# Kernel tuning notes

Measured on AMD Instinct MI355X. Metric: run time of the kernel, lower is better.

The kernel has to match this reference:

```python
import jax, jax.numpy as jnp
import numpy as np

B, T, H, L, OUT = 64, 2048, 256, 2, 256


def setup_inputs() -> dict:
    key = jax.random.key(0)
    ks = jax.random.split(key, 7)
    s = 1.0 / np.sqrt(H)
    return {
        "x": jax.random.normal(ks[0], (B, T, H), dtype=jnp.float32),
        "W_ih": jax.random.uniform(ks[1], (L, 4 * H, H), jnp.float32, -s, s),
        "W_hh": jax.random.uniform(ks[2], (L, 4 * H, H), jnp.float32, -s, s),
        "b_ih": jax.random.uniform(ks[3], (L, 4 * H), jnp.float32, -s, s),
        "b_hh": jax.random.uniform(ks[4], (L, 4 * H), jnp.float32, -s, s),
        "W_fc": jax.random.uniform(ks[5], (OUT, H), jnp.float32, -s, s),
        "b_fc": jax.random.uniform(ks[6], (OUT,), jnp.float32, -s, s),
    }


def _lstm_forward(x, W_ih, W_hh, b_ih, b_hh, W_fc, b_fc):
    n_layers = W_ih.shape[0]
    batch = x.shape[0]
    hidden = W_hh.shape[2]
    h0 = jnp.zeros((n_layers, batch, hidden), x.dtype)
    c0 = jnp.zeros((n_layers, batch, hidden), x.dtype)

    def step(carry, x_t):
        h, c = carry  # [L, B, H] each
        inp = x_t  # [B, in]
        new_h, new_c = [], []
        for l in range(n_layers):
            # gates: [B, 4H] = x W_ih^T + b_ih + h W_hh^T + b_hh
            gates = (inp @ W_ih[l].T + b_ih[l]) + (h[l] @ W_hh[l].T + b_hh[l])
            i_g, f_g, g_g, o_g = jnp.split(gates, 4, axis=-1)
            c_new = jax.nn.sigmoid(f_g) * c[l] + jax.nn.sigmoid(i_g) * jnp.tanh(g_g)
            h_new = jax.nn.sigmoid(o_g) * jnp.tanh(c_new)
            new_h.append(h_new)
            new_c.append(c_new)
            inp = h_new
        return (jnp.stack(new_h), jnp.stack(new_c)), None

    (h_T, _), _ = jax.lax.scan(step, (h0, c0), jnp.swapaxes(x, 0, 1))
    # fc applied to last timestep's top-layer hidden state
    return h_T[-1] @ W_fc.T + b_fc  # [B, OUT]


def reference(x, W_ih, W_hh, b_ih, b_hh, W_fc, b_fc):
    return _lstm_forward(x, W_ih, W_hh, b_ih, b_hh, W_fc, b_fc)
```

## Files before the change

### kernel.cpp

```cpp
#include <hip/hip_runtime.h>
#include <math.h>

typedef unsigned long long u64;
typedef __attribute__((ext_vector_type(8))) short short8v;
typedef __attribute__((ext_vector_type(4))) float f32x4;
typedef __attribute__((ext_vector_type(4))) unsigned uint4v;

#define LB 64
#define LT 2048
#define LH 256
#define LOUT 256
#define NWG 256

#define WS_CNT    0
#define WS_CNT_SZ ((size_t)8 * 16 * 16 * sizeof(int))
#define WS_H1     (64 * 1024)
#define WS_H2     (WS_H1 + 256 * 1024)
#define WS_BIAS   (WS_H2 + 256 * 1024)
#define WS_WT2    (1024 * 1024)
#define HBYTES    (256 * 1024)

#define MFMA(a, b, c) __builtin_amdgcn_mfma_f32_16x16x32_bf16(a, b, c, 0, 0, 0)
#define LD_IC(p) __hip_atomic_load((p), __ATOMIC_RELAXED, __HIP_MEMORY_SCOPE_AGENT)
#define ST_IC(p, v) __hip_atomic_store((p), (v), __ATOMIC_RELAXED, __HIP_MEMORY_SCOPE_AGENT)

__device__ __host__ __forceinline__ short bf16_rne(float f) {
    unsigned u = __builtin_bit_cast(unsigned, f);
    unsigned r = (u + 0x7fffu + ((u >> 16) & 1u)) >> 16;
    return (short)r;
}
__device__ __forceinline__ float bf16_to_f(short s) {
    unsigned u = ((unsigned)(unsigned short)s) << 16;
    return __builtin_bit_cast(float, u);
}
__device__ __forceinline__ float fsigm(float g) {
    return __builtin_amdgcn_rcpf(1.f + __builtin_amdgcn_exp2f(g * -1.44269504f));
}
__device__ __forceinline__ float ftanh(float g) {
    return __builtin_amdgcn_rcpf(1.f + __builtin_amdgcn_exp2f(g * -2.88539008f)) * 2.f - 1.f;
}

__global__ void prep_weights(const float* __restrict__ W_ih,
                             const float* __restrict__ W_hh,
                             const float* __restrict__ b_ih,
                             const float* __restrict__ b_hh,
                             unsigned short* __restrict__ Wt2,
                             float* __restrict__ bias_r) {
    int gid = blockIdx.x * 256 + threadIdx.x;
    if (gid >= (1 << 20)) return;
    int j   = gid & 7;
    int rwi = (gid >> 3) & 15;
    int kgi = (gid >> 7) & 3;
    int ks  = (gid >> 9) & 15;
    int mt  = (gid >> 13) & 3;
    int s   = (gid >> 15) & 15;
    int layer = gid >> 19;
    int k   = ks * 32 + kgi * 8 + j;
    int row = mt * 256 + s * 16 + rwi;
    float w = (k < 256) ? W_ih[((size_t)layer * 1024 + row) * 256 + k]
                        : W_hh[((size_t)layer * 1024 + row) * 256 + (k - 256)];
    short hi = bf16_rne(w);
    float rem = w - bf16_to_f(hi);
    short lo = bf16_rne(rem);
    size_t base = (((size_t)((layer * 16 + s) * 4 + mt) * 16 + ks) * 1024)
                  + (size_t)kgi * 128 + rwi * 8 + j;
    Wt2[base]       = (unsigned short)hi;
    Wt2[base + 512] = (unsigned short)lo;
    if (k == 0) {
        int ridx = s * 64 + mt * 16 + rwi;
        bias_r[layer * 1024 + ridx] = b_ih[layer * 1024 + row] + b_hh[layer * 1024 + row];
    }
}

__global__ __launch_bounds__(256, 1)
void lstm_persistent(const float* __restrict__ x,
                     const unsigned short* __restrict__ Wt2,
                     const float* __restrict__ bias_r,
                     char* __restrict__ h1c, char* __restrict__ h2c,
                     int* __restrict__ cnt)
{
    __shared__ __align__(16) f32x4 red[2][12][64];

    const int tid   = threadIdx.x;
    const int wg    = blockIdx.x;
    const int layer = wg >> 7;
    const int g     = wg & 127;
    const int bg    = g & 7;
    const int s     = g >> 3;
    const int b0    = bg * 8;
    const int wave  = tid >> 6;
    const int lane  = tid & 63;
    const int kg    = lane >> 4;
    const int rw    = lane & 15;
    const int rb    = rw & 7;
    const int batch = b0 + rb;
    int* const flags = cnt + bg * 256;

    short8v Ahi[4][4], Alo[4][4];
    #pragma unroll
    for (int mt = 0; mt < 4; ++mt)
        #pragma unroll
        for (int k2 = 0; k2 < 4; ++k2) {
            size_t base = (((size_t)((layer * 16 + s) * 4 + mt) * 16 + (wave * 4 + k2)) * 1024)
                          + (size_t)kg * 128 + rw * 8;
            Ahi[mt][k2] = *(const short8v*)((const short*)Wt2 + base);
            Alo[mt][k2] = *(const short8v*)((const short*)Wt2 + base + 512);
        }

    f32x4 biasv[4];
    #pragma unroll
    for (int mt = 0; mt < 4; ++mt)
        biasv[mt] = *(const f32x4*)(bias_r + layer * 1024 + s * 64 + mt * 16 + kg * 4);

    f32x4 creg = {0.f, 0.f, 0.f, 0.f};

    float4 xr[4][2];
    if (layer == 0 && wave < 2) {
        #pragma unroll
        for (int k2 = 0; k2 < 4; ++k2) {
            const int kbase = (wave * 4 + k2) * 32 + kg * 8;
            const float* xp = x + ((size_t)batch * LT + 0) * LH + kbase;
            xr[k2][0] = *(const float4*)xp;
            xr[k2][1] = *(const float4*)(xp + 4);
        }
    }

    for (int r = 0; r <= LT; ++r) {
        const bool active = (layer == 0) ? (r < LT) : (r >= 1);
        const int t = (layer == 0) ? r : (r - 1);

        short8v Bhi[4], Blo[4];
        bool useB = false;
        if (active) {
            if (layer == 0 && wave < 2) {
                #pragma unroll
                for (int k2 = 0; k2 < 4; ++k2) {
                    float fv[8] = {xr[k2][0].x, xr[k2][0].y, xr[k2][0].z, xr[k2][0].w,
                                   xr[k2][1].x, xr[k2][1].y, xr[k2][1].z, xr[k2][1].w};
                    short8v bh, bl;
                    #pragma unroll
                    for (int j = 0; j < 8; ++j) {
                        short hb = bf16_rne(fv[j]);
                        bh[j] = hb;
                        bl[j] = bf16_rne(fv[j] - bf16_to_f(hb));
                    }
                    Bhi[k2] = bh; Blo[k2] = bl;
                }
                useB = true;
            } else {
                const char* hbuf; int slot, kofs, tg; bool any;
                if (layer == 0)      { any = (t > 0); hbuf = h1c; slot = (t - 1) & 3; kofs = -256; tg = ((t - 1) >> 2) & 1; }
                else if (wave < 2)   { any = true;    hbuf = h1c; slot = t & 3;       kofs = 0;    tg = (t >> 2) & 1; }
                else                 { any = (t > 0); hbuf = h2c; slot = (t - 1) & 3; kofs = -256; tg = ((t - 1) >> 2) & 1; }
                if (any) {
                    u64 a0, a1, a2, a3;
                    {
                        int hb0 = (wave * 4 + 0) * 32 + kg * 8 + kofs;
                        int hb1 = hb0 + 32, hb2 = hb0 + 64, hb3 = hb0 + 96;
                        a0 = (u64)(hbuf + (size_t)((((slot * 64 + batch) * 16) + (hb0 >> 4)) * 4 + ((hb0 >> 2) & 3)) * 16);
                        a1 = (u64)(hbuf + (size_t)((((slot * 64 + batch) * 16) + (hb1 >> 4)) * 4 + ((hb1 >> 2) & 3)) * 16);
                        a2 = (u64)(hbuf + (size_t)((((slot * 64 + batch) * 16) + (hb2 >> 4)) * 4 + ((hb2 >> 2) & 3)) * 16);
                        a3 = (u64)(hbuf + (size_t)((((slot * 64 + batch) * 16) + (hb3 >> 4)) * 4 + ((hb3 >> 2) & 3)) * 16);
                    }
                    const unsigned m = 0x00010001u;
                    const unsigned wnt = tg ? 0x00010001u : 0u;
                    uint4v U0, U1, U2, U3, U4, U5, U6, U7;
                    for (;;) {
                        asm volatile(
                            "global_load_dwordx4 %0, %8, off sc0 sc1\n\t"
                            "global_load_dwordx4 %1, %8, off offset:16 sc0 sc1\n\t"
                            "global_load_dwordx4 %2, %9, off sc0 sc1\n\t"
                            "global_load_dwordx4 %3, %9, off offset:16 sc0 sc1\n\t"
                            "global_load_dwordx4 %4, %10, off sc0 sc1\n\t"
                            "global_load_dwordx4 %5, %10, off offset:16 sc0 sc1\n\t"
                            "global_load_dwordx4 %6, %11, off sc0 sc1\n\t"
                            "global_load_dwordx4 %7, %11, off offset:16 sc0 sc1\n\t"
                            "s_waitcnt vmcnt(0)"
                            : "=v"(U0), "=v"(U1), "=v"(U2), "=v"(U3),
                              "=v"(U4), "=v"(U5), "=v"(U6), "=v"(U7)
                            : "v"(a0), "v"(a1), "v"(a2), "v"(a3)
                            : "memory");
                        unsigned bad = ((U0.z & m) ^ wnt) | ((U0.w & m) ^ wnt)
                                     | ((U1.z & m) ^ wnt) | ((U1.w & m) ^ wnt)
                                     | ((U2.z & m) ^ wnt) | ((U2.w & m) ^ wnt)
                                     | ((U3.z & m) ^ wnt) | ((U3.w & m) ^ wnt)
                                     | ((U4.z & m) ^ wnt) | ((U4.w & m) ^ wnt)
                                     | ((U5.z & m) ^ wnt) | ((U5.w & m) ^ wnt)
                                     | ((U6.z & m) ^ wnt) | ((U6.w & m) ^ wnt)
                                     | ((U7.z & m) ^ wnt) | ((U7.w & m) ^ wnt);
                        if (__all(bad == 0u)) break;
                        __builtin_amdgcn_s_sleep(1);
                    }
                    union { unsigned d[4]; short8v v; } bh, bl;
                    bh.d[0] = U0.x; bh.d[1] = U0.y; bh.d[2] = U1.x; bh.d[3] = U1.y; Bhi[0] = bh.v;
                    bl.d[0] = U0.z; bl.d[1] = U0.w; bl.d[2] = U1.z; bl.d[3] = U1.w; Blo[0] = bl.v;
                    bh.d[0] = U2.x; bh.d[1] = U2.y; bh.d[2] = U3.x; bh.d[3] = U3.y; Bhi[1] = bh.v;
                    bl.d[0] = U2.z; bl.d[1] = U2.w; bl.d[2] = U3.z; bl.d[3] = U3.w; Blo[1] = bl.v;
                    bh.d[0] = U4.x; bh.d[1] = U4.y; bh.d[2] = U5.x; bh.d[3] = U5.y; Bhi[2] = bh.v;
                    bl.d[0] = U4.z; bl.d[1] = U4.w; bl.d[2] = U5.z; bl.d[3] = U5.w; Blo[2] = bl.v;
                    bh.d[0] = U6.x; bh.d[1] = U6.y; bh.d[2] = U7.x; bh.d[3] = U7.y; Bhi[3] = bh.v;
                    bl.d[0] = U6.z; bl.d[1] = U6.w; bl.d[2] = U7.z; bl.d[3] = U7.w; Blo[3] = bl.v;
                    useB = true;
                }
            }
        }

        f32x4 acc[4];
        #pragma unroll
        for (int mt = 0; mt < 4; ++mt) acc[mt] = (f32x4){0.f, 0.f, 0.f, 0.f};
        if (useB) {
            #pragma unroll
            for (int k2 = 0; k2 < 4; ++k2)
                #pragma unroll
                for (int mt = 0; mt < 4; ++mt) {
                    acc[mt] = MFMA(Ahi[mt][k2], Bhi[k2], acc[mt]);
                    acc[mt] = MFMA(Ahi[mt][k2], Blo[k2], acc[mt]);
                    acc[mt] = MFMA(Alo[mt][k2], Bhi[k2], acc[mt]);
                }
        }

        if (active && wave > 0) {
            #pragma unroll
            for (int mt = 0; mt < 4; ++mt) red[r & 1][(wave - 1) * 4 + mt][lane] = acc[mt];
        }
        __syncthreads();

        if (layer == 1 && wave == 0 && lane == 0)
            ST_IC(flags + s * 16, r + 1);

        if (active && wave == 0) {
            f32x4 gate[4];
            #pragma unroll
            for (int mt = 0; mt < 4; ++mt) {
                f32x4 gs = acc[mt] + biasv[mt];
                #pragma unroll
                for (int w = 0; w < 3; ++w) gs += red[r & 1][w * 4 + mt][lane];
                gate[mt] = gs;
            }
            float hv[4];
            #pragma unroll
            for (int rr = 0; rr < 4; ++rr) {
                float si = fsigm(gate[0][rr]);
                float sf = fsigm(gate[1][rr]);
                float so = fsigm(gate[3][rr]);
                float gg = ftanh(gate[2][rr]);
                float cn = sf * creg[rr] + si * gg;
                creg[rr] = cn;
                hv[rr] = so * ftanh(cn);
            }
            if (layer == 0) {
                const int tgt = r - 2;
                const int* fp = flags + (lane & 15) * 16;
                for (;;) {
                    int v = (lane < 16) ? LD_IC(fp) : 0x7fffffff;
                    if (__all(v >= tgt)) break;
                    __builtin_amdgcn_s_sleep(1);
                }
            }
            if (rw < 8) {
                const unsigned tgo = (unsigned)((t >> 2) & 1);
                u64 qh = 0, ql = 0;
                #pragma unroll
                for (int rr = 0; rr < 4; ++rr) {
                    unsigned short hb = (unsigned short)bf16_rne(hv[rr]);
                    unsigned short lb = (unsigned short)bf16_rne(hv[rr] - bf16_to_f((short)hb));
                    lb = (unsigned short)((lb & ~1u) | tgo);
                    qh |= ((u64)hb) << (16 * rr);
                    ql |= ((u64)lb) << (16 * rr);
                }
                uint4v dd;
                dd.x = (unsigned)qh; dd.y = (unsigned)(qh >> 32);
                dd.z = (unsigned)ql; dd.w = (unsigned)(ql >> 32);
                char* hbuf = (layer == 0 ? h1c : h2c);
                int unit = (((t & 3) * 64 + (b0 + rw)) * 16 + s) * 4 + kg;
                u64 ad = (u64)(hbuf + (size_t)unit * 16);
                asm volatile("global_store_dwordx4 %0, %1, off sc0 sc1"
                             :: "v"(ad), "v"(dd) : "memory");
            }
        }

        if (layer == 0 && wave < 2 && t + 1 < LT) {
            #pragma unroll
            for (int k2 = 0; k2 < 4; ++k2) {
                const int kbase = (wave * 4 + k2) * 32 + kg * 8;
                const float* xp = x + ((size_t)batch * LT + (t + 1)) * LH + kbase;
                xr[k2][0] = *(const float4*)xp;
                xr[k2][1] = *(const float4*)(xp + 4);
            }
        }
    }
}

__global__ __launch_bounds__(256)
void fc_kernel(const char* __restrict__ h2c,
               const float* __restrict__ W_fc,
               const float* __restrict__ b_fc,
               float* __restrict__ out) {
    int b = blockIdx.x;
    int o = threadIdx.x;
    __shared__ float hrow[LH];
    for (int k = threadIdx.x; k < LH; k += 256) {
        int unit = ((3 * 64 + b) * 16 + (k >> 4)) * 4 + ((k >> 2) & 3);
        const u64* up = (const u64*)(h2c + (size_t)unit * 16);
        u64 qh = up[0];
        u64 ql = up[1] & ~0x0001000100010001ULL;
        int sh = (k & 3) * 16;
        hrow[k] = bf16_to_f((short)(qh >> sh)) + bf16_to_f((short)(ql >> sh));
    }
    __syncthreads();
    float acc = b_fc[o];
#pragma unroll 8
    for (int k = 0; k < LH; ++k)
        acc = fmaf(W_fc[o * LH + k], hrow[k], acc);
    out[b * LOUT + o] = acc;
}

extern "C" void kernel_launch(void* const* d_in, const int* in_sizes, int n_in,
                              void* d_out, int out_size, void* d_ws, size_t ws_size,
                              hipStream_t stream) {
    const float* x    = (const float*)d_in[0];
    const float* W_ih = (const float*)d_in[1];
    const float* W_hh = (const float*)d_in[2];
    const float* b_ih = (const float*)d_in[3];
    const float* b_hh = (const float*)d_in[4];
    const float* W_fc = (const float*)d_in[5];
    const float* b_fc = (const float*)d_in[6];
    float* out = (float*)d_out;

    char* ws = (char*)d_ws;
    int*            cnt    = (int*)(ws + WS_CNT);
    char*           h1c    = ws + WS_H1;
    char*           h2c    = ws + WS_H2;
    float*          bias_r = (float*)(ws + WS_BIAS);
    unsigned short* Wt2    = (unsigned short*)(ws + WS_WT2);

    hipMemsetAsync(cnt, 0, WS_CNT_SZ, stream);
    hipMemsetAsync(h1c, 0xFF, HBYTES, stream);
    hipMemsetAsync(h2c, 0xFF, HBYTES, stream);
    prep_weights<<<(1 << 20) / 256, 256, 0, stream>>>(W_ih, W_hh, b_ih, b_hh, Wt2, bias_r);

    void* args[] = {(void*)&x, (void*)&Wt2, (void*)&bias_r,
                    (void*)&h1c, (void*)&h2c, (void*)&cnt};
    hipError_t e = hipLaunchCooperativeKernel(lstm_persistent, dim3(NWG), dim3(256),
                                              args, 0, stream);
    if (e != hipSuccess) {
        lstm_persistent<<<NWG, 256, 0, stream>>>(x, Wt2, bias_r, h1c, h2c, cnt);
    }

    fc_kernel<<<LB, 256, 0, stream>>>(h2c, W_fc, b_fc, out);
}
```

Before: 9.317 ms.

## Replace data-embedded toggle polling with XCC-aware flag barriers and local-cache loads

After: 8.370 ms. -10.2%, faster.

```diff
diff --git a/kernel.cpp b/kernel.cpp
--- a/kernel.cpp
+++ b/kernel.cpp
@@ -13,16 +13,14 @@
 #define NWG 256
 
 #define WS_CNT    0
-#define WS_CNT_SZ ((size_t)8 * 16 * 16 * sizeof(int))
+#define WS_CNT_SZ (12 * 1024)
+#define TICK_OFF  2048
 #define WS_H1     (64 * 1024)
 #define WS_H2     (WS_H1 + 256 * 1024)
 #define WS_BIAS   (WS_H2 + 256 * 1024)
 #define WS_WT2    (1024 * 1024)
-#define HBYTES    (256 * 1024)
 
 #define MFMA(a, b, c) __builtin_amdgcn_mfma_f32_16x16x32_bf16(a, b, c, 0, 0, 0)
-#define LD_IC(p) __hip_atomic_load((p), __ATOMIC_RELAXED, __HIP_MEMORY_SCOPE_AGENT)
-#define ST_IC(p, v) __hip_atomic_store((p), (v), __ATOMIC_RELAXED, __HIP_MEMORY_SCOPE_AGENT)
 
 __device__ __host__ __forceinline__ short bf16_rne(float f) {
     unsigned u = __builtin_bit_cast(unsigned, f);
@@ -38,6 +36,59 @@
 }
 __device__ __forceinline__ float ftanh(float g) {
     return __builtin_amdgcn_rcpf(1.f + __builtin_amdgcn_exp2f(g * -2.88539008f)) * 2.f - 1.f;
+}
+
+template <int LOCAL>
+__device__ __forceinline__ int ld_flag(const int* p) {
+    int v; u64 a = (u64)p;
+    if (LOCAL) asm volatile("global_load_dword %0, %1, off sc0\n\ts_waitcnt vmcnt(0)"
+                            : "=&v"(v) : "v"(a) : "memory");
+    else       asm volatile("global_load_dword %0, %1, off sc0 sc1\n\ts_waitcnt vmcnt(0)"
+                            : "=&v"(v) : "v"(a) : "memory");
+    return v;
+}
+template <int LOCAL>
+__device__ __forceinline__ void st_flag(int* p, int v) {
+    u64 a = (u64)p;
+    if (LOCAL) asm volatile("global_store_dword %0, %1, off sc0" :: "v"(a), "v"(v) : "memory");
+    else       asm volatile("global_store_dword %0, %1, off sc0 sc1" :: "v"(a), "v"(v) : "memory");
+}
+template <int LOCAL>
+__device__ __forceinline__ void st_unit(void* p, uint4v d) {
+    u64 a = (u64)p;
+    if (LOCAL) asm volatile("global_store_dwordx4 %0, %1, off sc0" :: "v"(a), "v"(d) : "memory");
+    else       asm volatile("global_store_dwordx4 %0, %1, off sc0 sc1" :: "v"(a), "v"(d) : "memory");
+}
+template <int LOCAL>
+__device__ __forceinline__ void ld_units(u64 a0, u64 a1, u64 a2, u64 a3,
+        uint4v& U0, uint4v& U1, uint4v& U2, uint4v& U3,
+        uint4v& U4, uint4v& U5, uint4v& U6, uint4v& U7) {
+    if (LOCAL) asm volatile(
+        "global_load_dwordx4 %0, %8, off sc0\n\t"
+        "global_load_dwordx4 %1, %8, off offset:16 sc0\n\t"
+        "global_load_dwordx4 %2, %9, off sc0\n\t"
+        "global_load_dwordx4 %3, %9, off offset:16 sc0\n\t"
+        "global_load_dwordx4 %4, %10, off sc0\n\t"
+        "global_load_dwordx4 %5, %10, off offset:16 sc0\n\t"
+        "global_load_dwordx4 %6, %11, off sc0\n\t"
+        "global_load_dwordx4 %7, %11, off offset:16 sc0\n\t"
+        "s_waitcnt vmcnt(0)"
+        : "=&v"(U0), "=&v"(U1), "=&v"(U2), "=&v"(U3),
+          "=&v"(U4), "=&v"(U5), "=&v"(U6), "=&v"(U7)
+        : "v"(a0), "v"(a1), "v"(a2), "v"(a3) : "memory");
+    else asm volatile(
+        "global_load_dwordx4 %0, %8, off sc0 sc1\n\t"
+        "global_load_dwordx4 %1, %8, off offset:16 sc0 sc1\n\t"
+        "global_load_dwordx4 %2, %9, off sc0 sc1\n\t"
+        "global_load_dwordx4 %3, %9, off offset:16 sc0 sc1\n\t"
+        "global_load_dwordx4 %4, %10, off sc0 sc1\n\t"
+        "global_load_dwordx4 %5, %10, off offset:16 sc0 sc1\n\t"
+        "global_load_dwordx4 %6, %11, off sc0 sc1\n\t"
+        "global_load_dwordx4 %7, %11, off offset:16 sc0 sc1\n\t"
+        "s_waitcnt vmcnt(0)"
+        : "=&v"(U0), "=&v"(U1), "=&v"(U2), "=&v"(U3),
+          "=&v"(U4), "=&v"(U5), "=&v"(U6), "=&v"(U7)
+        : "v"(a0), "v"(a1), "v"(a2), "v"(a3) : "memory");
 }
 
 __global__ void prep_weights(const float* __restrict__ W_ih,
@@ -79,22 +130,49 @@
                      char* __restrict__ h1c, char* __restrict__ h2c,
                      int* __restrict__ cnt)
 {
-    __shared__ __align__(16) f32x4 red[2][12][64];
+    __shared__ __align__(16) f32x4 red[12][64];
+    __shared__ int s_mode, s_bg, s_role;
 
     const int tid   = threadIdx.x;
-    const int wg    = blockIdx.x;
-    const int layer = wg >> 7;
-    const int g     = wg & 127;
-    const int bg    = g & 7;
-    const int s     = g >> 3;
-    const int b0    = bg * 8;
     const int wave  = tid >> 6;
     const int lane  = tid & 63;
+
+    if (tid == 0) {
+        unsigned xcc = (unsigned)__builtin_amdgcn_s_getreg(20 | (3 << 11)) & 7u;
+        int* tick = cnt + TICK_OFF;
+        int tk = __hip_atomic_fetch_add(tick + xcc, 1, __ATOMIC_RELAXED, __HIP_MEMORY_SCOPE_AGENT);
+        __hip_atomic_fetch_add(tick + 8, 1, __ATOMIC_RELEASE, __HIP_MEMORY_SCOPE_AGENT);
+        while (__hip_atomic_load(tick + 8, __ATOMIC_ACQUIRE, __HIP_MEMORY_SCOPE_AGENT) < NWG)
+            __builtin_amdgcn_s_sleep(8);
+        int bal = 1;
+        for (int i = 0; i < 8; ++i)
+            bal &= (__hip_atomic_load(tick + i, __ATOMIC_RELAXED, __HIP_MEMORY_SCOPE_AGENT) == 32);
+        s_mode = bal;
+        s_bg   = bal ? (int)xcc : (int)(blockIdx.x & 7);
+        s_role = bal ? tk : (int)(((blockIdx.x >> 7) << 4) | ((blockIdx.x & 127) >> 3));
+    }
+    __syncthreads();
+
+    __builtin_amdgcn_fence(__ATOMIC_SEQ_CST, "agent");
+    __syncthreads();
+    if (tid == 0) {
+        int* b2 = cnt + TICK_OFF + 16;
+        __hip_atomic_fetch_add(b2, 1, __ATOMIC_RELEASE, __HIP_MEMORY_SCOPE_AGENT);
+        while (__hip_atomic_load(b2, __ATOMIC_ACQUIRE, __HIP_MEMORY_SCOPE_AGENT) < NWG)
+            __builtin_amdgcn_s_sleep(8);
+    }
+    __syncthreads();
+
+    const int mode  = s_mode;
+    const int bg    = s_bg;
+    const int layer = s_role >> 4;
+    const int s     = s_role & 15;
+    const int b0    = bg * 8;
     const int kg    = lane >> 4;
     const int rw    = lane & 15;
     const int rb    = rw & 7;
     const int batch = b0 + rb;
-    int* const flags = cnt + bg * 256;
+    int* const fl_base = cnt + bg * 256;
 
     short8v Ahi[4][4], Alo[4][4];
     #pragma unroll
@@ -148,49 +226,23 @@
                 }
                 useB = true;
             } else {
-                const char* hbuf; int slot, kofs, tg; bool any;
-                if (layer == 0)      { any = (t > 0); hbuf = h1c; slot = (t - 1) & 3; kofs = -256; tg = ((t - 1) >> 2) & 1; }
-                else if (wave < 2)   { any = true;    hbuf = h1c; slot = t & 3;       kofs = 0;    tg = (t >> 2) & 1; }
-                else                 { any = (t > 0); hbuf = h2c; slot = (t - 1) & 3; kofs = -256; tg = ((t - 1) >> 2) & 1; }
+                const char* hbuf; int slot, kofs; bool any;
+                if (layer == 0)      { any = (t > 0); hbuf = h1c; slot = (t - 1) & 3; kofs = -256; }
+                else if (wave < 2)   { any = true;    hbuf = h1c; slot = t & 3;       kofs = 0;    }
+                else                 { any = (t > 0); hbuf = h2c; slot = (t - 1) & 3; kofs = -256; }
                 if (any) {
+                    const int kb0 = wave * 128 + kg * 8 + kofs;
                     u64 a0, a1, a2, a3;
                     {
-                        int hb0 = (wave * 4 + 0) * 32 + kg * 8 + kofs;
-                        int hb1 = hb0 + 32, hb2 = hb0 + 64, hb3 = hb0 + 96;
-                        a0 = (u64)(hbuf + (size_t)((((slot * 64 + batch) * 16) + (hb0 >> 4)) * 4 + ((hb0 >> 2) & 3)) * 16);
-                        a1 = (u64)(hbuf + (size_t)((((slot * 64 + batch) * 16) + (hb1 >> 4)) * 4 + ((hb1 >> 2) & 3)) * 16);
-                        a2 = (u64)(hbuf + (size_t)((((slot * 64 + batch) * 16) + (hb2 >> 4)) * 4 + ((hb2 >> 2) & 3)) * 16);
-                        a3 = (u64)(hbuf + (size_t)((((slot * 64 + batch) * 16) + (hb3 >> 4)) * 4 + ((hb3 >> 2) & 3)) * 16);
+                        int kb;
+                        kb = kb0;       a0 = (u64)(hbuf + (size_t)((((slot * 64 + batch) * 16) + (kb >> 4)) * 4 + ((kb >> 2) & 3)) * 16);
+                        kb = kb0 + 32;  a1 = (u64)(hbuf + (size_t)((((slot * 64 + batch) * 16) + (kb >> 4)) * 4 + ((kb >> 2) & 3)) * 16);
+                        kb = kb0 + 64;  a2 = (u64)(hbuf + (size_t)((((slot * 64 + batch) * 16) + (kb >> 4)) * 4 + ((kb >> 2) & 3)) * 16);
+                        kb = kb0 + 96;  a3 = (u64)(hbuf + (size_t)((((slot * 64 + batch) * 16) + (kb >> 4)) * 4 + ((kb >> 2) & 3)) * 16);
                     }
-                    const unsigned m = 0x00010001u;
-                    const unsigned wnt = tg ? 0x00010001u : 0u;
                     uint4v U0, U1, U2, U3, U4, U5, U6, U7;
-                    for (;;) {
-                        asm volatile(
-                            "global_load_dwordx4 %0, %8, off sc0 sc1\n\t"
-                            "global_load_dwordx4 %1, %8, off offset:16 sc0 sc1\n\t"
-                            "global_load_dwordx4 %2, %9, off sc0 sc1\n\t"
-                            "global_load_dwordx4 %3, %9, off offset:16 sc0 sc1\n\t"
-                            "global_load_dwordx4 %4, %10, off sc0 sc1\n\t"
-                            "global_load_dwordx4 %5, %10, off offset:16 sc0 sc1\n\t"
-                            "global_load_dwordx4 %6, %11, off sc0 sc1\n\t"
-                            "global_load_dwordx4 %7, %11, off offset:16 sc0 sc1\n\t"
-                            "s_waitcnt vmcnt(0)"
-                            : "=v"(U0), "=v"(U1), "=v"(U2), "=v"(U3),
-                              "=v"(U4), "=v"(U5), "=v"(U6), "=v"(U7)
-                            : "v"(a0), "v"(a1), "v"(a2), "v"(a3)
-                            : "memory");
-                        unsigned bad = ((U0.z & m) ^ wnt) | ((U0.w & m) ^ wnt)
-                                     | ((U1.z & m) ^ wnt) | ((U1.w & m) ^ wnt)
-                                     | ((U2.z & m) ^ wnt) | ((U2.w & m) ^ wnt)
-                                     | ((U3.z & m) ^ wnt) | ((U3.w & m) ^ wnt)
-                                     | ((U4.z & m) ^ wnt) | ((U4.w & m) ^ wnt)
-                                     | ((U5.z & m) ^ wnt) | ((U5.w & m) ^ wnt)
-                                     | ((U6.z & m) ^ wnt) | ((U6.w & m) ^ wnt)
-                                     | ((U7.z & m) ^ wnt) | ((U7.w & m) ^ wnt);
-                        if (__all(bad == 0u)) break;
-                        __builtin_amdgcn_s_sleep(1);
-                    }
+                    if (mode) ld_units<1>(a0, a1, a2, a3, U0, U1, U2, U3, U4, U5, U6, U7);
+                    else      ld_units<0>(a0, a1, a2, a3, U0, U1, U2, U3, U4, U5, U6, U7);
                     union { unsigned d[4]; short8v v; } bh, bl;
                     bh.d[0] = U0.x; bh.d[1] = U0.y; bh.d[2] = U1.x; bh.d[3] = U1.y; Bhi[0] = bh.v;
                     bl.d[0] = U0.z; bl.d[1] = U0.w; bl.d[2] = U1.z; bl.d[3] = U1.w; Blo[0] = bl.v;
@@ -221,12 +273,9 @@
 
         if (active && wave > 0) {
             #pragma unroll
-            for (int mt = 0; mt < 4; ++mt) red[r & 1][(wave - 1) * 4 + mt][lane] = acc[mt];
+            for (int mt = 0; mt < 4; ++mt) red[(wave - 1) * 4 + mt][lane] = acc[mt];
         }
         __syncthreads();
-
-        if (layer == 1 && wave == 0 && lane == 0)
-            ST_IC(flags + s * 16, r + 1);
 
         if (active && wave == 0) {
             f32x4 gate[4];
@@ -234,7 +283,7 @@
             for (int mt = 0; mt < 4; ++mt) {
                 f32x4 gs = acc[mt] + biasv[mt];
                 #pragma unroll
-                for (int w = 0; w < 3; ++w) gs += red[r & 1][w * 4 + mt][lane];
+                for (int w = 0; w < 3; ++w) gs += red[w * 4 + mt][lane];
                 gate[mt] = gs;
             }
             float hv[4];
@@ -248,23 +297,12 @@
                 creg[rr] = cn;
                 hv[rr] = so * ftanh(cn);
             }
-            if (layer == 0) {
-                const int tgt = r - 2;
-                const int* fp = flags + (lane & 15) * 16;
-                for (;;) {
-                    int v = (lane < 16) ? LD_IC(fp) : 0x7fffffff;
-                    if (__all(v >= tgt)) break;
-                    __builtin_amdgcn_s_sleep(1);
-                }
-            }
             if (rw < 8) {
-                const unsigned tgo = (unsigned)((t >> 2) & 1);
                 u64 qh = 0, ql = 0;
                 #pragma unroll
                 for (int rr = 0; rr < 4; ++rr) {
                     unsigned short hb = (unsigned short)bf16_rne(hv[rr]);
                     unsigned short lb = (unsigned short)bf16_rne(hv[rr] - bf16_to_f((short)hb));
-                    lb = (unsigned short)((lb & ~1u) | tgo);
                     qh |= ((u64)hb) << (16 * rr);
                     ql |= ((u64)lb) << (16 * rr);
                 }
@@ -273,9 +311,17 @@
                 dd.z = (unsigned)ql; dd.w = (unsigned)(ql >> 32);
                 char* hbuf = (layer == 0 ? h1c : h2c);
                 int unit = (((t & 3) * 64 + (b0 + rw)) * 16 + s) * 4 + kg;
-                u64 ad = (u64)(hbuf + (size_t)unit * 16);
-                asm volatile("global_store_dwordx4 %0, %1, off sc0 sc1"
-                             :: "v"(ad), "v"(dd) : "memory");
+                if (mode) st_unit<1>(hbuf + (size_t)unit * 16, dd);
+                else      st_unit<0>(hbuf + (size_t)unit * 16, dd);
+            }
+        }
+
+        if (wave == 0 && r < LT) {
+            asm volatile("s_waitcnt vmcnt(0)" ::: "memory");
+            if (lane == 0) {
+                int* fp = fl_base + (layer * 16 + s) * 16;
+                if (mode) { st_flag<1>(fp, r + 1); st_flag<0>(fp, r + 1); }
+                else      st_flag<0>(fp, r + 1);
             }
         }
 
@@ -287,6 +333,26 @@
                 xr[k2][0] = *(const float4*)xp;
                 xr[k2][1] = *(const float4*)(xp + 4);
             }
+        }
+
+        if (r < LT) {
+            if (wave == 0) {
+                const int mL  = lane >> 4;
+                const int tgt = (layer == 0) ? ((mL == 0) ? r + 1 : r - 1) : (r + 1);
+                int* fp = fl_base + (lane & 31) * 16;
+                int it = 0;
+                for (;;) {
+                    int v = 0x7fffffff;
+                    if (lane < 32) {
+                        ++it;
+                        if (mode && (it & 7) != 0) v = ld_flag<1>(fp);
+                        else                       v = ld_flag<0>(fp);
+                    }
+                    if (__all(v >= tgt)) break;
+                    if (!mode) __builtin_amdgcn_s_sleep(1);
+                }
+            }
+            __syncthreads();
         }
     }
 }
@@ -303,7 +369,7 @@
         int unit = ((3 * 64 + b) * 16 + (k >> 4)) * 4 + ((k >> 2) & 3);
         const u64* up = (const u64*)(h2c + (size_t)unit * 16);
         u64 qh = up[0];
-        u64 ql = up[1] & ~0x0001000100010001ULL;
+        u64 ql = up[1];
         int sh = (k & 3) * 16;
         hrow[k] = bf16_to_f((short)(qh >> sh)) + bf16_to_f((short)(ql >> sh));
     }
@@ -335,8 +401,6 @@
     unsigned short* Wt2    = (unsigned short*)(ws + WS_WT2);
 
     hipMemsetAsync(cnt, 0, WS_CNT_SZ, stream);
-    hipMemsetAsync(h1c, 0xFF, HBYTES, stream);
-    hipMemsetAsync(h2c, 0xFF, HBYTES, stream);
     prep_weights<<<(1 << 20) / 256, 256, 0, stream>>>(W_ih, W_hh, b_ih, b_hh, Wt2, bias_r);
 
     void* args[] = {(void*)&x, (void*)&Wt2, (void*)&bias_r,
```
